# Kernel tuning notes

Hardware: AMD Instinct MI355X
Metric: run time of the kernel (lower is better)

## Reference

```python
import jax, jax.numpy as jnp
import numpy as np

N = 100000   # num_nodes
E = 1600000  # num_edges
D = 32       # hidden dim
H = 2        # GAT heads
EF = 16      # edge_feat_dim


def setup_inputs() -> dict:
    key = jax.random.key(0)
    ks = jax.random.split(key, 18)
    s = 0.1
    inp = {
        "edge_index": jax.random.randint(ks[0], (2, E), 0, N),
        "edge_attr": jax.random.normal(ks[1], (E, EF), jnp.float32),
        "node_emb": jax.random.normal(ks[2], (N, D), jnp.float32) * s,
        # SAGEConv layers: lin_l (neighbors, with bias) + lin_r (root, no bias)
        "sage1_wl": jax.random.normal(ks[3], (D, D), jnp.float32) * s,
        "sage1_bl": jnp.zeros((D,), jnp.float32),
        "sage1_wr": jax.random.normal(ks[4], (D, D), jnp.float32) * s,
        "sage2_wl": jax.random.normal(ks[5], (D, D), jnp.float32) * s,
        "sage2_bl": jnp.zeros((D,), jnp.float32),
        "sage2_wr": jax.random.normal(ks[6], (D, D), jnp.float32) * s,
        # GATConv: lin (no bias), att_src/att_dst [H, D], output bias [D]
        "gat_w": jax.random.normal(ks[7], (D, H * D), jnp.float32) * s,
        "gat_att_src": jax.random.normal(ks[8], (H, D), jnp.float32) * s,
        "gat_att_dst": jax.random.normal(ks[9], (H, D), jnp.float32) * s,
        "gat_bias": jnp.zeros((D,), jnp.float32),
        # edge MLP: Linear(2D+EF, 32) -> ReLU -> Linear(32, 1)
        "mlp_w1": jax.random.normal(ks[10], (2 * D + EF, 32), jnp.float32) * s,
        "mlp_b1": jnp.zeros((32,), jnp.float32),
        "mlp_w2": jax.random.normal(ks[11], (32, 1), jnp.float32) * s,
        "mlp_b2": jnp.zeros((1,), jnp.float32),
    }
    return inp


def _sage(x, src, dst, wl, bl, wr):
    # mean aggregation of source messages at destination, then lin_l + lin_r(root)
    summ = jax.ops.segment_sum(x[src], dst, num_segments=N)
    cnt = jax.ops.segment_sum(jnp.ones((src.shape[0], 1), x.dtype), dst, num_segments=N)
    mean = summ / jnp.maximum(cnt, 1.0)
    return mean @ wl + bl + x @ wr


def _gat(x, src, dst, w, att_src, att_dst, bias):
    # PyG GATConv default: add self loops, softmax over incoming edges per dst,
    # concat=False -> mean over heads, then bias.
    loops = jnp.arange(N, dtype=src.dtype)
    s2 = jnp.concatenate([src, loops])
    d2 = jnp.concatenate([dst, loops])
    xh = (x @ w).reshape(N, H, D)                      # [N, H, D]
    a_s = jnp.einsum('nhd,hd->nh', xh, att_src)        # [N, H]
    a_d = jnp.einsum('nhd,hd->nh', xh, att_dst)
    alpha = jax.nn.leaky_relu(a_s[s2] + a_d[d2], 0.2)  # [E+N, H]
    m = jax.ops.segment_max(alpha, d2, num_segments=N)
    e = jnp.exp(alpha - m[d2])
    den = jax.ops.segment_sum(e, d2, num_segments=N)
    wgt = e / (den[d2] + 1e-16)                        # [E+N, H]
    out = jax.ops.segment_sum(xh[s2] * wgt[:, :, None], d2, num_segments=N)
    return out.mean(axis=1) + bias                     # [N, D]


def reference(edge_index, edge_attr, node_emb,
              sage1_wl, sage1_bl, sage1_wr,
              sage2_wl, sage2_bl, sage2_wr,
              gat_w, gat_att_src, gat_att_dst, gat_bias,
              mlp_w1, mlp_b1, mlp_w2, mlp_b2):
    src, dst = edge_index[0], edge_index[1]
    x = node_emb
    x = jax.nn.relu(_sage(x, src, dst, sage1_wl, sage1_bl, sage1_wr))
    x = jax.nn.relu(_sage(x, src, dst, sage2_wl, sage2_bl, sage2_wr))
    x = jax.nn.relu(_gat(x, src, dst, gat_w, gat_att_src, gat_att_dst, gat_bias))
    edge_input = jnp.concatenate([x[src], x[dst], edge_attr], axis=1)  # [E, 2D+EF]
    h = jax.nn.relu(edge_input @ mlp_w1 + mlp_b1)  # dropout is eval-mode identity
    return (h @ mlp_w2 + mlp_b2).squeeze()         # [E]
```

## Files before the change

### kernel.cpp

```cpp
#include <hip/hip_runtime.h>
#include <hip/hip_fp16.h>


#define DD 32
#define HH 2
#define EFF 16

#define EB 4096
#define PB_T 512
#define BIN_SHIFT 8

__device__ __forceinline__ float lrelu(float x) { return x > 0.f ? x : 0.2f * x; }

__global__ void scan1_k(const int* __restrict__ in, int* __restrict__ out,
                        int* __restrict__ blockSums, int M) {
    __shared__ int s_s[256];
    int blk = blockIdx.x, t = threadIdx.x;
    int base = blk * 1024 + t * 4;
    int v[4];
    int s = 0;
#pragma unroll
    for (int i = 0; i < 4; i++) {
        v[i] = (base + i < M) ? in[base + i] : 0;
        s += v[i];
    }
    s_s[t] = s;
    __syncthreads();
    for (int off = 1; off < 256; off <<= 1) {
        int x = (t >= off) ? s_s[t - off] : 0;
        __syncthreads();
        s_s[t] += x;
        __syncthreads();
    }
    int excl = s_s[t] - s;
#pragma unroll
    for (int i = 0; i < 4; i++) {
        if (base + i < M) out[base + i] = excl;
        excl += v[i];
    }
    if (t == 255) blockSums[blk] = s_s[255];
}

__global__ void scan2_k(int* __restrict__ blockSums, int* __restrict__ totalOut, int NB) {
    __shared__ int s_s[256];
    int t = threadIdx.x;
    int v = (t < NB) ? blockSums[t] : 0;
    s_s[t] = v;
    __syncthreads();
    for (int off = 1; off < 256; off <<= 1) {
        int x = (t >= off) ? s_s[t - off] : 0;
        __syncthreads();
        s_s[t] += x;
        __syncthreads();
    }
    if (t < NB) blockSums[t] = s_s[t] - v;
    if (t == 255) *totalOut = s_s[255];
}

__global__ void scan3_k(int* __restrict__ out, const int* __restrict__ blockSums, int M) {
    int i = blockIdx.x * blockDim.x + threadIdx.x;
    if (i < M) out[i] += blockSums[i >> 10];
}

__global__ void radixA_k(const int* __restrict__ dst, int* __restrict__ histA, int E,
                         int NBLK, int NBINS) {
    __shared__ int s_h[512];
    int blk = blockIdx.x, t = threadIdx.x;
    for (int b = t; b < 512; b += PB_T) s_h[b] = 0;
    __syncthreads();
    int e0 = blk * EB;
    for (int i = t; i < EB; i += PB_T) {
        int e = e0 + i;
        if (e < E) atomicAdd(&s_h[dst[e] >> BIN_SHIFT], 1);
    }
    __syncthreads();
    for (int b = t; b < NBINS; b += PB_T) histA[b * NBLK + blk] = s_h[b];
}

__global__ void radixB_k(const int* __restrict__ src, const int* __restrict__ dst,
                         const int* __restrict__ histScan, int* __restrict__ pairs,
                         int E, int NBLK, int NBINS) {
    __shared__ int s_base[512];
    int blk = blockIdx.x, t = threadIdx.x;
    for (int b = t; b < NBINS; b += PB_T) s_base[b] = histScan[b * NBLK + blk];
    __syncthreads();
    int e0 = blk * EB;
    for (int i = t; i < EB; i += PB_T) {
        int e = e0 + i;
        if (e < E) {
            int d = dst[e];
            int pos = atomicAdd(&s_base[d >> BIN_SHIFT], 1);
            pairs[pos] = (src[e] << 8) | (d & 255);
        }
    }
}

__global__ void radixC_v2(const int* __restrict__ histScan, const int* __restrict__ pairs,
                          int* __restrict__ rowptr, int* __restrict__ soff, int N,
                          int NBLK, int NBINS, int E) {
    __shared__ int cnt[256];
    __shared__ int scanBuf[256];
    __shared__ int basePos[256];
    int b = blockIdx.x, t = threadIdx.x;
    int base = b << BIN_SHIFT;
    cnt[t] = 0;
    __syncthreads();
    int segLo = histScan[b * NBLK];
    int segHi = (b + 1 < NBINS) ? histScan[(b + 1) * NBLK] : E;
    for (int i = segLo + t; i < segHi; i += 256) atomicAdd(&cnt[pairs[i] & 255], 1);
    __syncthreads();
    int v = cnt[t];
    scanBuf[t] = v;
    __syncthreads();
    for (int off = 1; off < 256; off <<= 1) {
        int x = (t >= off) ? scanBuf[t - off] : 0;
        __syncthreads();
        scanBuf[t] += x;
        __syncthreads();
    }
    int excl = segLo + scanBuf[t] - v;
    basePos[t] = excl;
    if (base + t < N) rowptr[base + t] = excl;
    if (b == NBINS - 1 && t == 0) rowptr[N] = E;
    __syncthreads();
    for (int i = segLo + t; i < segHi; i += 256) {
        int en = pairs[i];
        int pos = atomicAdd(&basePos[en & 255], 1);
        soff[pos] = (en >> 8) << 6;
    }
}

__global__ void cvt_k(const float* __restrict__ in, __half* __restrict__ out, int n) {
    int i = blockIdx.x * blockDim.x + threadIdx.x;
    if (i < n) out[i] = __float2half(in[i]);
}

__global__ void prep_c_k(const float* __restrict__ w, const float* __restrict__ att_src,
                         const float* __restrict__ att_dst, float4* __restrict__ c4) {
    int i = threadIdx.x;
    if (i >= DD) return;
    float cs0 = 0.f, cs1 = 0.f, cd0 = 0.f, cd1 = 0.f;
    for (int d = 0; d < DD; d++) {
        float w0 = w[i * (HH * DD) + d], w1 = w[i * (HH * DD) + DD + d];
        cs0 += w0 * att_src[d];
        cs1 += w1 * att_src[DD + d];
        cd0 += w0 * att_dst[d];
        cd1 += w1 * att_dst[DD + d];
    }
    c4[i] = make_float4(cs0, cs1, cd0, cd1);
}

__device__ __forceinline__ void unpack4(unsigned lo, unsigned hi, float f[4]) {
    float2 a = __half22float2(*reinterpret_cast<const __half2*>(&lo));
    float2 b = __half22float2(*reinterpret_cast<const __half2*>(&hi));
    f[0] = a.x; f[1] = a.y; f[2] = b.x; f[3] = b.y;
}

__global__ void sage8x8_k(const __half* __restrict__ x, const int* __restrict__ rowptr,
                          const int* __restrict__ soff, const float* __restrict__ wl,
                          const float* __restrict__ bl, const float* __restrict__ wr,
                          __half* __restrict__ out, const float4* __restrict__ c4,
                          float2* __restrict__ a_s, float2* __restrict__ a_d, int N) {
    __shared__ float s_wl[DD * DD];
    __shared__ float s_wr[DD * DD];
    __shared__ float s_b[DD];
    __shared__ float4 s_c[DD];
    for (int i = threadIdx.x; i < DD * DD; i += blockDim.x) {
        s_wl[i] = wl[i];
        s_wr[i] = wr[i];
    }
    if (threadIdx.x < DD) {
        s_b[threadIdx.x] = bl[threadIdx.x];
        if (a_s) s_c[threadIdx.x] = c4[threadIdx.x];
    }
    __syncthreads();
    int gid = blockIdx.x * blockDim.x + threadIdx.x;
    int n = gid >> 3;
    if (n >= N) return;
    int l = gid & 7;
    int lo = rowptr[n], hi = rowptr[n + 1];
    const char* xb = (const char*)x;
    float acc[4] = {0.f, 0.f, 0.f, 0.f};
    int j = lo;
    for (; j + 3 < hi; j += 4) {
        int o0 = soff[j], o1 = soff[j + 1], o2 = soff[j + 2], o3 = soff[j + 3];
        uint2 r0 = *(const uint2*)(xb + o0 + l * 8);
        uint2 r1 = *(const uint2*)(xb + o1 + l * 8);
        uint2 r2 = *(const uint2*)(xb + o2 + l * 8);
        uint2 r3 = *(const uint2*)(xb + o3 + l * 8);
        float v0[4], v1[4], v2[4], v3[4];
        unpack4(r0.x, r0.y, v0);
        unpack4(r1.x, r1.y, v1);
        unpack4(r2.x, r2.y, v2);
        unpack4(r3.x, r3.y, v3);
#pragma unroll
        for (int f = 0; f < 4; f++) acc[f] += (v0[f] + v1[f]) + (v2[f] + v3[f]);
    }
    for (; j < hi; j++) {
        uint2 r0 = *(const uint2*)(xb + soff[j] + l * 8);
        float v0[4];
        unpack4(r0.x, r0.y, v0);
#pragma unroll
        for (int f = 0; f < 4; f++) acc[f] += v0[f];
    }
    float inv = 1.0f / fmaxf((float)(hi - lo), 1.0f);
    float mx[4];
#pragma unroll
    for (int f = 0; f < 4; f++) mx[f] = acc[f] * inv;
    uint2 sr = *(const uint2*)(xb + (size_t)n * 64 + l * 8);
    float xv[4];
    unpack4(sr.x, sr.y, xv);
    float o[4];
#pragma unroll
    for (int f = 0; f < 4; f++) o[f] = s_b[4 * l + f];
#pragma unroll
    for (int i2 = 0; i2 < 8; i2++) {
        float bm[4], bx[4];
#pragma unroll
        for (int r = 0; r < 4; r++) {
            bm[r] = __shfl(mx[r], i2, 8);
            bx[r] = __shfl(xv[r], i2, 8);
        }
#pragma unroll
        for (int r = 0; r < 4; r++) {
            const float4 wlv = *(const float4*)(s_wl + (4 * i2 + r) * DD + 4 * l);
            const float4 wrv = *(const float4*)(s_wr + (4 * i2 + r) * DD + 4 * l);
            o[0] += bm[r] * wlv.x + bx[r] * wrv.x;
            o[1] += bm[r] * wlv.y + bx[r] * wrv.y;
            o[2] += bm[r] * wlv.z + bx[r] * wrv.z;
            o[3] += bm[r] * wlv.w + bx[r] * wrv.w;
        }
    }
#pragma unroll
    for (int f = 0; f < 4; f++) o[f] = fmaxf(o[f], 0.f);
    uint2 ow;
    *reinterpret_cast<__half2*>(&ow.x) = __floats2half2_rn(o[0], o[1]);
    *reinterpret_cast<__half2*>(&ow.y) = __floats2half2_rn(o[2], o[3]);
    *(uint2*)((char*)out + (size_t)n * 64 + l * 8) = ow;
    if (a_s) {
        float pa0 = 0.f, pa1 = 0.f, pd0 = 0.f, pd1 = 0.f;
#pragma unroll
        for (int r = 0; r < 4; r++) {
            float4 c = s_c[4 * l + r];
            pa0 += o[r] * c.x;
            pa1 += o[r] * c.y;
            pd0 += o[r] * c.z;
            pd1 += o[r] * c.w;
        }
#pragma unroll
        for (int off = 4; off > 0; off >>= 1) {
            pa0 += __shfl_xor(pa0, off, 8);
            pa1 += __shfl_xor(pa1, off, 8);
            pd0 += __shfl_xor(pd0, off, 8);
            pd1 += __shfl_xor(pd1, off, 8);
        }
        if (l == 0) {
            a_s[n] = make_float2(pa0, pa1);
            a_d[n] = make_float2(pd0, pd1);
        }
    }
}

__global__ void gat_agg_v10(const __half* __restrict__ x2, const float2* __restrict__ a_s,
                            const float2* __restrict__ a_d, const int* __restrict__ rowptr,
                            const int* __restrict__ soff, const float* __restrict__ gw,
                            const float* __restrict__ bias, const float* __restrict__ w1,
                            const float* __restrict__ b1, __half* __restrict__ Ps,
                            __half* __restrict__ Pd, int N) {
    __shared__ float s_gw[DD * HH * DD];
    __shared__ float s_w1[2 * DD * DD];
    __shared__ float s_b1[DD];
    __shared__ float s_bias[DD];
    int t = threadIdx.x;
    for (int i = t; i < DD * HH * DD; i += blockDim.x) s_gw[i] = gw[i];
    for (int i = t; i < 2 * DD * DD; i += blockDim.x) s_w1[i] = w1[i];
    if (t < DD) {
        s_b1[t] = b1[t];
        s_bias[t] = bias[t];
    }
    __syncthreads();
    int gid = blockIdx.x * blockDim.x + t;
    int n = gid >> 3;
    if (n >= N) return;
    int l = gid & 7;
    const char* xb = (const char*)x2;
    const char* asb = (const char*)a_s;
    int lo = rowptr[n], hi = rowptr[n + 1];
    float2 as = a_s[n], ad = a_d[n];
    float ws0 = __expf(lrelu(as.x + ad.x));
    float ws1 = __expf(lrelu(as.y + ad.y));
    uint2 sr = *(const uint2*)(xb + (size_t)n * 64 + l * 8);
    float xvs[4];
    unpack4(sr.x, sr.y, xvs);
    float den0 = ws0, den1 = ws1;
    float y0[4], y1[4];
#pragma unroll
    for (int f = 0; f < 4; f++) {
        y0[f] = ws0 * xvs[f];
        y1[f] = ws1 * xvs[f];
    }
    int j = lo;
    for (; j + 3 < hi; j += 4) {
        int o0 = soff[j], o1 = soff[j + 1], o2 = soff[j + 2], o3 = soff[j + 3];
        float2 s0 = *(const float2*)(asb + (o0 >> 3));
        float2 s1 = *(const float2*)(asb + (o1 >> 3));
        float2 s2 = *(const float2*)(asb + (o2 >> 3));
        float2 s3 = *(const float2*)(asb + (o3 >> 3));
        uint2 r0 = *(const uint2*)(xb + o0 + l * 8);
        uint2 r1 = *(const uint2*)(xb + o1 + l * 8);
        uint2 r2 = *(const uint2*)(xb + o2 + l * 8);
        uint2 r3 = *(const uint2*)(xb + o3 + l * 8);
        float w00 = __expf(lrelu(s0.x + ad.x)), w01 = __expf(lrelu(s0.y + ad.y));
        float w10 = __expf(lrelu(s1.x + ad.x)), w11 = __expf(lrelu(s1.y + ad.y));
        float w20 = __expf(lrelu(s2.x + ad.x)), w21 = __expf(lrelu(s2.y + ad.y));
        float w30 = __expf(lrelu(s3.x + ad.x)), w31 = __expf(lrelu(s3.y + ad.y));
        den0 += (w00 + w10) + (w20 + w30);
        den1 += (w01 + w11) + (w21 + w31);
        float v0[4], v1[4], v2[4], v3[4];
        unpack4(r0.x, r0.y, v0);
        unpack4(r1.x, r1.y, v1);
        unpack4(r2.x, r2.y, v2);
        unpack4(r3.x, r3.y, v3);
#pragma unroll
        for (int f = 0; f < 4; f++) {
            y0[f] += (w00 * v0[f] + w10 * v1[f]) + (w20 * v2[f] + w30 * v3[f]);
            y1[f] += (w01 * v0[f] + w11 * v1[f]) + (w21 * v2[f] + w31 * v3[f]);
        }
    }
    for (; j < hi; j++) {
        int o0 = soff[j];
        float2 s0 = *(const float2*)(asb + (o0 >> 3));
        uint2 r0 = *(const uint2*)(xb + o0 + l * 8);
        float w00 = __expf(lrelu(s0.x + ad.x)), w01 = __expf(lrelu(s0.y + ad.y));
        den0 += w00;
        den1 += w01;
        float v0[4];
        unpack4(r0.x, r0.y, v0);
#pragma unroll
        for (int f = 0; f < 4; f++) {
            y0[f] += w00 * v0[f];
            y1[f] += w01 * v0[f];
        }
    }
    float i0 = 1.0f / (den0 + 1e-16f), i1 = 1.0f / (den1 + 1e-16f);
    float u0[4], u1[4];
#pragma unroll
    for (int f = 0; f < 4; f++) {
        u0[f] = y0[f] * i0;
        u1[f] = y1[f] * i1;
    }
    float o[4] = {0.f, 0.f, 0.f, 0.f};
#pragma unroll
    for (int i2 = 0; i2 < 8; i2++) {
        float b0[4], b1v[4];
#pragma unroll
        for (int r = 0; r < 4; r++) {
            b0[r] = __shfl(u0[r], i2, 8);
            b1v[r] = __shfl(u1[r], i2, 8);
        }
#pragma unroll
        for (int r = 0; r < 4; r++) {
            const float4 g0 = *(const float4*)(s_gw + (4 * i2 + r) * (HH * DD) + 4 * l);
            const float4 g1 = *(const float4*)(s_gw + (4 * i2 + r) * (HH * DD) + DD + 4 * l);
            o[0] += b0[r] * g0.x + b1v[r] * g1.x;
            o[1] += b0[r] * g0.y + b1v[r] * g1.y;
            o[2] += b0[r] * g0.z + b1v[r] * g1.z;
            o[3] += b0[r] * g0.w + b1v[r] * g1.w;
        }
    }
#pragma unroll
    for (int f = 0; f < 4; f++) o[f] = fmaxf(0.5f * o[f] + s_bias[4 * l + f], 0.f);
    float ps[4], pd[4];
#pragma unroll
    for (int f = 0; f < 4; f++) {
        ps[f] = s_b1[4 * l + f];
        pd[f] = 0.f;
    }
#pragma unroll
    for (int i2 = 0; i2 < 8; i2++) {
        float bo[4];
#pragma unroll
        for (int r = 0; r < 4; r++) bo[r] = __shfl(o[r], i2, 8);
#pragma unroll
        for (int r = 0; r < 4; r++) {
            const float4 wa = *(const float4*)(s_w1 + (4 * i2 + r) * DD + 4 * l);
            const float4 wb = *(const float4*)(s_w1 + (DD + 4 * i2 + r) * DD + 4 * l);
            ps[0] += bo[r] * wa.x;
            ps[1] += bo[r] * wa.y;
            ps[2] += bo[r] * wa.z;
            ps[3] += bo[r] * wa.w;
            pd[0] += bo[r] * wb.x;
            pd[1] += bo[r] * wb.y;
            pd[2] += bo[r] * wb.z;
            pd[3] += bo[r] * wb.w;
        }
    }
    uint2 pw;
    *reinterpret_cast<__half2*>(&pw.x) = __floats2half2_rn(ps[0], ps[1]);
    *reinterpret_cast<__half2*>(&pw.y) = __floats2half2_rn(ps[2], ps[3]);
    *(uint2*)((char*)Ps + (size_t)n * 64 + l * 8) = pw;
    *reinterpret_cast<__half2*>(&pw.x) = __floats2half2_rn(pd[0], pd[1]);
    *reinterpret_cast<__half2*>(&pw.y) = __floats2half2_rn(pd[2], pd[3]);
    *(uint2*)((char*)Pd + (size_t)n * 64 + l * 8) = pw;
}

__device__ __forceinline__ void add_half_row(const __half* __restrict__ row, float acc[DD]) {
    const uint4* r4 = (const uint4*)row;
#pragma unroll
    for (int c = 0; c < 4; c++) {
        uint4 u = r4[c];
        unsigned uu[4] = {u.x, u.y, u.z, u.w};
#pragma unroll
        for (int t = 0; t < 4; t++) {
            __half2 h2 = *reinterpret_cast<const __half2*>(&uu[t]);
            float2 f = __half22float2(h2);
            acc[c * 8 + t * 2 + 0] += f.x;
            acc[c * 8 + t * 2 + 1] += f.y;
        }
    }
}

__global__ void edge_mlp_v3(const __half* __restrict__ Ps, const __half* __restrict__ Pd,
                            const float* __restrict__ eattr, const int* __restrict__ src,
                            const int* __restrict__ dst, const float* __restrict__ w1e,
                            const float* __restrict__ w2, const float* __restrict__ b2,
                            float* __restrict__ out, int E) {
    __shared__ float s_we[EFF * DD];
    __shared__ float s_w2[DD];
    for (int i = threadIdx.x; i < EFF * DD; i += blockDim.x) s_we[i] = w1e[i];
    if (threadIdx.x < DD) s_w2[threadIdx.x] = w2[threadIdx.x];
    __syncthreads();
    int e = blockIdx.x * blockDim.x + threadIdx.x;
    if (e >= E) return;
    float b2v = b2[0];
    int s = src[e], d = dst[e];
    float acc[DD] = {};
    add_half_row(Ps + (size_t)s * DD, acc);
    add_half_row(Pd + (size_t)d * DD, acc);
    const float4* ea4 = (const float4*)(eattr + (size_t)e * EFF);
#pragma unroll
    for (int c = 0; c < 4; c++) {
        float4 v = ea4[c];
        const float va[4] = {v.x, v.y, v.z, v.w};
#pragma unroll
        for (int r = 0; r < 4; r++) {
#pragma unroll
            for (int j4 = 0; j4 < 8; j4++) {
                const float4 w = *(const float4*)(s_we + (c * 4 + r) * DD + j4 * 4);
                acc[j4 * 4 + 0] += va[r] * w.x;
                acc[j4 * 4 + 1] += va[r] * w.y;
                acc[j4 * 4 + 2] += va[r] * w.z;
                acc[j4 * 4 + 3] += va[r] * w.w;
            }
        }
    }
    float p = b2v;
#pragma unroll
    for (int j = 0; j < DD; j++) p += fmaxf(acc[j], 0.f) * s_w2[j];
    out[e] = p;
}

extern "C" void kernel_launch(void* const* d_in, const int* in_sizes, int n_in,
                              void* d_out, int out_size, void* d_ws, size_t ws_size,
                              hipStream_t stream) {
    const int E = in_sizes[0] / 2;
    const int N = in_sizes[2] / DD;

    const int* src = (const int*)d_in[0];
    const int* dst = src + E;
    const float* edge_attr = (const float*)d_in[1];
    const float* node_emb = (const float*)d_in[2];
    const float* sage1_wl = (const float*)d_in[3];
    const float* sage1_bl = (const float*)d_in[4];
    const float* sage1_wr = (const float*)d_in[5];
    const float* sage2_wl = (const float*)d_in[6];
    const float* sage2_bl = (const float*)d_in[7];
    const float* sage2_wr = (const float*)d_in[8];
    const float* gat_w = (const float*)d_in[9];
    const float* gat_att_src = (const float*)d_in[10];
    const float* gat_att_dst = (const float*)d_in[11];
    const float* gat_bias = (const float*)d_in[12];
    const float* mlp_w1 = (const float*)d_in[13];
    const float* mlp_b1 = (const float*)d_in[14];
    const float* mlp_w2 = (const float*)d_in[15];
    const float* mlp_b2 = (const float*)d_in[16];
    float* out = (float*)d_out;

    const int NBINS = (N + 255) >> BIN_SHIFT;
    const int NBLK = (E + EB - 1) / EB;
    const int M = NBINS * NBLK;

    char* ws = (char*)d_ws;
    size_t off = 0;
    auto alloc = [&](size_t bytes) {
        char* p = ws + off;
        off = (off + bytes + 255) & ~(size_t)255;
        return p;
    };
    int* rowptr = (int*)alloc((size_t)(N + 1) * 4);
    int* blockSums = (int*)alloc(256 * 4);
    int* dTot = (int*)alloc(4);
    int* soff = (int*)alloc((size_t)E * 4);
    __half* x0h = (__half*)alloc((size_t)N * DD * 2);
    __half* x1h = (__half*)alloc((size_t)N * DD * 2);
    __half* x2h = (__half*)alloc((size_t)N * DD * 2);
    float2* a_s = (float2*)alloc((size_t)N * 8);
    float2* a_d = (float2*)alloc((size_t)N * 8);
    float4* c4 = (float4*)alloc(DD * 16);
    __half* Ps = (__half*)alloc((size_t)N * DD * 2);
    __half* Pd = (__half*)alloc((size_t)N * DD * 2);
    int* histA = (int*)alloc((size_t)M * 4);
    int* histScan = (int*)alloc((size_t)M * 4);
    int* pairs = (int*)alloc((size_t)E * 4);

    const int BS = 256;
    const int gE = (E + BS - 1) / BS;
    const int gN32 = (N * 32 + BS - 1) / BS;
    const int gN8 = (N * 8 + BS - 1) / BS;
    const int NBm = (M + 1023) / 1024;

    radixA_k<<<NBLK, PB_T, 0, stream>>>(dst, histA, E, NBLK, NBINS);
    scan1_k<<<NBm, 256, 0, stream>>>(histA, histScan, blockSums, M);
    scan2_k<<<1, 256, 0, stream>>>(blockSums, dTot, NBm);
    scan3_k<<<(M + BS - 1) / BS, BS, 0, stream>>>(histScan, blockSums, M);
    radixB_k<<<NBLK, PB_T, 0, stream>>>(src, dst, histScan, pairs, E, NBLK, NBINS);
    radixC_v2<<<NBINS, 256, 0, stream>>>(histScan, pairs, rowptr, soff, N, NBLK, NBINS, E);

    cvt_k<<<gN32, BS, 0, stream>>>(node_emb, x0h, N * DD);
    prep_c_k<<<1, 64, 0, stream>>>(gat_w, gat_att_src, gat_att_dst, c4);

    sage8x8_k<<<gN8, BS, 0, stream>>>(x0h, rowptr, soff, sage1_wl, sage1_bl, sage1_wr,
                                      x1h, nullptr, nullptr, nullptr, N);
    sage8x8_k<<<gN8, BS, 0, stream>>>(x1h, rowptr, soff, sage2_wl, sage2_bl, sage2_wr,
                                      x2h, c4, a_s, a_d, N);

    gat_agg_v10<<<gN8, BS, 0, stream>>>(x2h, a_s, a_d, rowptr, soff, gat_w, gat_bias,
                                        mlp_w1, mlp_b1, Ps, Pd, N);

    edge_mlp_v3<<<gE, BS, 0, stream>>>(Ps, Pd, edge_attr, src, dst,
                                       mlp_w1 + 2 * DD * DD, mlp_w2, mlp_b2, out, E);
}
```

Measured before the change: 253.3 us.

## Use 4 lanes per node with 16-byte loads; fp16 packed math in edge MLP

The SAGE and GAT aggregation kernels now give each node 4 lanes with 16-byte row loads instead of 8 lanes with 8-byte loads. This halves thread count and shuffle overhead, and each lane handles 8 features with 2-way unrolled neighbor loops. The edge MLP now does its accumulation in packed half2 FMAs, with the edge-attr weights converted to half in shared memory. The fp16 accumulation reduces precision of the hidden layer and risks tolerance failures, and the shorter unroll may expose more gather latency.

```diff
diff --git a/kernel.cpp b/kernel.cpp
--- a/kernel.cpp
+++ b/kernel.cpp
@@ -150,17 +150,20 @@
     c4[i] = make_float4(cs0, cs1, cd0, cd1);
 }
 
-__device__ __forceinline__ void unpack4(unsigned lo, unsigned hi, float f[4]) {
-    float2 a = __half22float2(*reinterpret_cast<const __half2*>(&lo));
-    float2 b = __half22float2(*reinterpret_cast<const __half2*>(&hi));
+__device__ __forceinline__ void unpack8(uint4 u, float f[8]) {
+    float2 a = __half22float2(*reinterpret_cast<const __half2*>(&u.x));
+    float2 b = __half22float2(*reinterpret_cast<const __half2*>(&u.y));
+    float2 c = __half22float2(*reinterpret_cast<const __half2*>(&u.z));
+    float2 d = __half22float2(*reinterpret_cast<const __half2*>(&u.w));
     f[0] = a.x; f[1] = a.y; f[2] = b.x; f[3] = b.y;
-}
-
-__global__ void sage8x8_k(const __half* __restrict__ x, const int* __restrict__ rowptr,
-                          const int* __restrict__ soff, const float* __restrict__ wl,
-                          const float* __restrict__ bl, const float* __restrict__ wr,
-                          __half* __restrict__ out, const float4* __restrict__ c4,
-                          float2* __restrict__ a_s, float2* __restrict__ a_d, int N) {
+    f[4] = c.x; f[5] = c.y; f[6] = d.x; f[7] = d.y;
+}
+
+__global__ void sage4x16_k(const __half* __restrict__ x, const int* __restrict__ rowptr,
+                           const int* __restrict__ soff, const float* __restrict__ wl,
+                           const float* __restrict__ bl, const float* __restrict__ wr,
+                           __half* __restrict__ out, const float4* __restrict__ c4,
+                           float2* __restrict__ a_s, float2* __restrict__ a_d, int N) {
     __shared__ float s_wl[DD * DD];
     __shared__ float s_wr[DD * DD];
     __shared__ float s_b[DD];
@@ -175,84 +178,85 @@
     }
     __syncthreads();
     int gid = blockIdx.x * blockDim.x + threadIdx.x;
-    int n = gid >> 3;
+    int n = gid >> 2;
     if (n >= N) return;
-    int l = gid & 7;
+    int l = gid & 3;
     int lo = rowptr[n], hi = rowptr[n + 1];
     const char* xb = (const char*)x;
-    float acc[4] = {0.f, 0.f, 0.f, 0.f};
+    float acc[8] = {};
     int j = lo;
-    for (; j + 3 < hi; j += 4) {
-        int o0 = soff[j], o1 = soff[j + 1], o2 = soff[j + 2], o3 = soff[j + 3];
-        uint2 r0 = *(const uint2*)(xb + o0 + l * 8);
-        uint2 r1 = *(const uint2*)(xb + o1 + l * 8);
-        uint2 r2 = *(const uint2*)(xb + o2 + l * 8);
-        uint2 r3 = *(const uint2*)(xb + o3 + l * 8);
-        float v0[4], v1[4], v2[4], v3[4];
-        unpack4(r0.x, r0.y, v0);
-        unpack4(r1.x, r1.y, v1);
-        unpack4(r2.x, r2.y, v2);
-        unpack4(r3.x, r3.y, v3);
-#pragma unroll
-        for (int f = 0; f < 4; f++) acc[f] += (v0[f] + v1[f]) + (v2[f] + v3[f]);
-    }
-    for (; j < hi; j++) {
-        uint2 r0 = *(const uint2*)(xb + soff[j] + l * 8);
-        float v0[4];
-        unpack4(r0.x, r0.y, v0);
-#pragma unroll
-        for (int f = 0; f < 4; f++) acc[f] += v0[f];
+    for (; j + 1 < hi; j += 2) {
+        int o0 = soff[j], o1 = soff[j + 1];
+        uint4 r0 = *(const uint4*)(xb + o0 + l * 16);
+        uint4 r1 = *(const uint4*)(xb + o1 + l * 16);
+        float v0[8], v1[8];
+        unpack8(r0, v0);
+        unpack8(r1, v1);
+#pragma unroll
+        for (int f = 0; f < 8; f++) acc[f] += v0[f] + v1[f];
+    }
+    if (j < hi) {
+        uint4 r0 = *(const uint4*)(xb + soff[j] + l * 16);
+        float v0[8];
+        unpack8(r0, v0);
+#pragma unroll
+        for (int f = 0; f < 8; f++) acc[f] += v0[f];
     }
     float inv = 1.0f / fmaxf((float)(hi - lo), 1.0f);
-    float mx[4];
-#pragma unroll
-    for (int f = 0; f < 4; f++) mx[f] = acc[f] * inv;
-    uint2 sr = *(const uint2*)(xb + (size_t)n * 64 + l * 8);
-    float xv[4];
-    unpack4(sr.x, sr.y, xv);
-    float o[4];
-#pragma unroll
-    for (int f = 0; f < 4; f++) o[f] = s_b[4 * l + f];
-#pragma unroll
-    for (int i2 = 0; i2 < 8; i2++) {
-        float bm[4], bx[4];
-#pragma unroll
-        for (int r = 0; r < 4; r++) {
-            bm[r] = __shfl(mx[r], i2, 8);
-            bx[r] = __shfl(xv[r], i2, 8);
-        }
-#pragma unroll
-        for (int r = 0; r < 4; r++) {
-            const float4 wlv = *(const float4*)(s_wl + (4 * i2 + r) * DD + 4 * l);
-            const float4 wrv = *(const float4*)(s_wr + (4 * i2 + r) * DD + 4 * l);
-            o[0] += bm[r] * wlv.x + bx[r] * wrv.x;
-            o[1] += bm[r] * wlv.y + bx[r] * wrv.y;
-            o[2] += bm[r] * wlv.z + bx[r] * wrv.z;
-            o[3] += bm[r] * wlv.w + bx[r] * wrv.w;
-        }
-    }
-#pragma unroll
-    for (int f = 0; f < 4; f++) o[f] = fmaxf(o[f], 0.f);
-    uint2 ow;
+    float mx[8];
+#pragma unroll
+    for (int f = 0; f < 8; f++) mx[f] = acc[f] * inv;
+    uint4 sr = *(const uint4*)(xb + (size_t)n * 64 + l * 16);
+    float xv[8];
+    unpack8(sr, xv);
+    float o[8];
+#pragma unroll
+    for (int f = 0; f < 8; f++) o[f] = s_b[8 * l + f];
+#pragma unroll
+    for (int i2 = 0; i2 < 4; i2++) {
+#pragma unroll
+        for (int r = 0; r < 8; r++) {
+            float bm = __shfl(mx[r], i2, 4);
+            float bx = __shfl(xv[r], i2, 4);
+            int row = 8 * i2 + r;
+            const float4 wl0 = *(const float4*)(s_wl + row * DD + 8 * l);
+            const float4 wl1 = *(const float4*)(s_wl + row * DD + 8 * l + 4);
+            const float4 wr0 = *(const float4*)(s_wr + row * DD + 8 * l);
+            const float4 wr1 = *(const float4*)(s_wr + row * DD + 8 * l + 4);
+            o[0] += bm * wl0.x + bx * wr0.x;
+            o[1] += bm * wl0.y + bx * wr0.y;
+            o[2] += bm * wl0.z + bx * wr0.z;
+            o[3] += bm * wl0.w + bx * wr0.w;
+            o[4] += bm * wl1.x + bx * wr1.x;
+            o[5] += bm * wl1.y + bx * wr1.y;
+            o[6] += bm * wl1.z + bx * wr1.z;
+            o[7] += bm * wl1.w + bx * wr1.w;
+        }
+    }
+#pragma unroll
+    for (int f = 0; f < 8; f++) o[f] = fmaxf(o[f], 0.f);
+    uint4 ow;
     *reinterpret_cast<__half2*>(&ow.x) = __floats2half2_rn(o[0], o[1]);
     *reinterpret_cast<__half2*>(&ow.y) = __floats2half2_rn(o[2], o[3]);
-    *(uint2*)((char*)out + (size_t)n * 64 + l * 8) = ow;
+    *reinterpret_cast<__half2*>(&ow.z) = __floats2half2_rn(o[4], o[5]);
+    *reinterpret_cast<__half2*>(&ow.w) = __floats2half2_rn(o[6], o[7]);
+    *(uint4*)((char*)out + (size_t)n * 64 + l * 16) = ow;
     if (a_s) {
         float pa0 = 0.f, pa1 = 0.f, pd0 = 0.f, pd1 = 0.f;
 #pragma unroll
-        for (int r = 0; r < 4; r++) {
-            float4 c = s_c[4 * l + r];
+        for (int r = 0; r < 8; r++) {
+            float4 c = s_c[8 * l + r];
             pa0 += o[r] * c.x;
             pa1 += o[r] * c.y;
             pd0 += o[r] * c.z;
             pd1 += o[r] * c.w;
         }
 #pragma unroll
-        for (int off = 4; off > 0; off >>= 1) {
-            pa0 += __shfl_xor(pa0, off, 8);
-            pa1 += __shfl_xor(pa1, off, 8);
-            pd0 += __shfl_xor(pd0, off, 8);
-            pd1 += __shfl_xor(pd1, off, 8);
+        for (int off = 2; off > 0; off >>= 1) {
+            pa0 += __shfl_xor(pa0, off, 4);
+            pa1 += __shfl_xor(pa1, off, 4);
+            pd0 += __shfl_xor(pd0, off, 4);
+            pd1 += __shfl_xor(pd1, off, 4);
         }
         if (l == 0) {
             a_s[n] = make_float2(pa0, pa1);
@@ -261,7 +265,7 @@
     }
 }
 
-__global__ void gat_agg_v10(const __half* __restrict__ x2, const float2* __restrict__ a_s,
+__global__ void gat_agg_v11(const __half* __restrict__ x2, const float2* __restrict__ a_s,
                             const float2* __restrict__ a_d, const int* __restrict__ rowptr,
                             const int* __restrict__ soff, const float* __restrict__ gw,
                             const float* __restrict__ bias, const float* __restrict__ w1,
@@ -280,183 +284,185 @@
     }
     __syncthreads();
     int gid = blockIdx.x * blockDim.x + t;
-    int n = gid >> 3;
+    int n = gid >> 2;
     if (n >= N) return;
-    int l = gid & 7;
+    int l = gid & 3;
     const char* xb = (const char*)x2;
     const char* asb = (const char*)a_s;
     int lo = rowptr[n], hi = rowptr[n + 1];
     float2 as = a_s[n], ad = a_d[n];
     float ws0 = __expf(lrelu(as.x + ad.x));
     float ws1 = __expf(lrelu(as.y + ad.y));
-    uint2 sr = *(const uint2*)(xb + (size_t)n * 64 + l * 8);
-    float xvs[4];
-    unpack4(sr.x, sr.y, xvs);
+    uint4 sr = *(const uint4*)(xb + (size_t)n * 64 + l * 16);
+    float xvs[8];
+    unpack8(sr, xvs);
     float den0 = ws0, den1 = ws1;
-    float y0[4], y1[4];
-#pragma unroll
-    for (int f = 0; f < 4; f++) {
+    float y0[8], y1[8];
+#pragma unroll
+    for (int f = 0; f < 8; f++) {
         y0[f] = ws0 * xvs[f];
         y1[f] = ws1 * xvs[f];
     }
     int j = lo;
-    for (; j + 3 < hi; j += 4) {
-        int o0 = soff[j], o1 = soff[j + 1], o2 = soff[j + 2], o3 = soff[j + 3];
+    for (; j + 1 < hi; j += 2) {
+        int o0 = soff[j], o1 = soff[j + 1];
         float2 s0 = *(const float2*)(asb + (o0 >> 3));
         float2 s1 = *(const float2*)(asb + (o1 >> 3));
-        float2 s2 = *(const float2*)(asb + (o2 >> 3));
-        float2 s3 = *(const float2*)(asb + (o3 >> 3));
-        uint2 r0 = *(const uint2*)(xb + o0 + l * 8);
-        uint2 r1 = *(const uint2*)(xb + o1 + l * 8);
-        uint2 r2 = *(const uint2*)(xb + o2 + l * 8);
-        uint2 r3 = *(const uint2*)(xb + o3 + l * 8);
+        uint4 r0 = *(const uint4*)(xb + o0 + l * 16);
+        uint4 r1 = *(const uint4*)(xb + o1 + l * 16);
         float w00 = __expf(lrelu(s0.x + ad.x)), w01 = __expf(lrelu(s0.y + ad.y));
         float w10 = __expf(lrelu(s1.x + ad.x)), w11 = __expf(lrelu(s1.y + ad.y));
-        float w20 = __expf(lrelu(s2.x + ad.x)), w21 = __expf(lrelu(s2.y + ad.y));
-        float w30 = __expf(lrelu(s3.x + ad.x)), w31 = __expf(lrelu(s3.y + ad.y));
-        den0 += (w00 + w10) + (w20 + w30);
-        den1 += (w01 + w11) + (w21 + w31);
-        float v0[4], v1[4], v2[4], v3[4];
-        unpack4(r0.x, r0.y, v0);
-        unpack4(r1.x, r1.y, v1);
-        unpack4(r2.x, r2.y, v2);
-        unpack4(r3.x, r3.y, v3);
-#pragma unroll
-        for (int f = 0; f < 4; f++) {
-            y0[f] += (w00 * v0[f] + w10 * v1[f]) + (w20 * v2[f] + w30 * v3[f]);
-            y1[f] += (w01 * v0[f] + w11 * v1[f]) + (w21 * v2[f] + w31 * v3[f]);
-        }
-    }
-    for (; j < hi; j++) {
+        den0 += w00 + w10;
+        den1 += w01 + w11;
+        float v0[8], v1[8];
+        unpack8(r0, v0);
+        unpack8(r1, v1);
+#pragma unroll
+        for (int f = 0; f < 8; f++) {
+            y0[f] += w00 * v0[f] + w10 * v1[f];
+            y1[f] += w01 * v0[f] + w11 * v1[f];
+        }
+    }
+    if (j < hi) {
         int o0 = soff[j];
         float2 s0 = *(const float2*)(asb + (o0 >> 3));
-        uint2 r0 = *(const uint2*)(xb + o0 + l * 8);
+        uint4 r0 = *(const uint4*)(xb + o0 + l * 16);
         float w00 = __expf(lrelu(s0.x + ad.x)), w01 = __expf(lrelu(s0.y + ad.y));
         den0 += w00;
         den1 += w01;
-        float v0[4];
-        unpack4(r0.x, r0.y, v0);
-#pragma unroll
-        for (int f = 0; f < 4; f++) {
+        float v0[8];
+        unpack8(r0, v0);
+#pragma unroll
+        for (int f = 0; f < 8; f++) {
             y0[f] += w00 * v0[f];
             y1[f] += w01 * v0[f];
         }
     }
     float i0 = 1.0f / (den0 + 1e-16f), i1 = 1.0f / (den1 + 1e-16f);
-    float u0[4], u1[4];
-#pragma unroll
-    for (int f = 0; f < 4; f++) {
+    float u0[8], u1[8];
+#pragma unroll
+    for (int f = 0; f < 8; f++) {
         u0[f] = y0[f] * i0;
         u1[f] = y1[f] * i1;
     }
-    float o[4] = {0.f, 0.f, 0.f, 0.f};
-#pragma unroll
-    for (int i2 = 0; i2 < 8; i2++) {
-        float b0[4], b1v[4];
-#pragma unroll
-        for (int r = 0; r < 4; r++) {
-            b0[r] = __shfl(u0[r], i2, 8);
-            b1v[r] = __shfl(u1[r], i2, 8);
-        }
-#pragma unroll
-        for (int r = 0; r < 4; r++) {
-            const float4 g0 = *(const float4*)(s_gw + (4 * i2 + r) * (HH * DD) + 4 * l);
-            const float4 g1 = *(const float4*)(s_gw + (4 * i2 + r) * (HH * DD) + DD + 4 * l);
-            o[0] += b0[r] * g0.x + b1v[r] * g1.x;
-            o[1] += b0[r] * g0.y + b1v[r] * g1.y;
-            o[2] += b0[r] * g0.z + b1v[r] * g1.z;
-            o[3] += b0[r] * g0.w + b1v[r] * g1.w;
-        }
-    }
-#pragma unroll
-    for (int f = 0; f < 4; f++) o[f] = fmaxf(0.5f * o[f] + s_bias[4 * l + f], 0.f);
-    float ps[4], pd[4];
-#pragma unroll
-    for (int f = 0; f < 4; f++) {
-        ps[f] = s_b1[4 * l + f];
+    float o[8] = {};
+#pragma unroll
+    for (int i2 = 0; i2 < 4; i2++) {
+#pragma unroll
+        for (int r = 0; r < 8; r++) {
+            float b0 = __shfl(u0[r], i2, 4);
+            float b1v = __shfl(u1[r], i2, 4);
+            int row = 8 * i2 + r;
+            const float4 g00 = *(const float4*)(s_gw + row * (HH * DD) + 8 * l);
+            const float4 g01 = *(const float4*)(s_gw + row * (HH * DD) + 8 * l + 4);
+            const float4 g10 = *(const float4*)(s_gw + row * (HH * DD) + DD + 8 * l);
+            const float4 g11 = *(const float4*)(s_gw + row * (HH * DD) + DD + 8 * l + 4);
+            o[0] += b0 * g00.x + b1v * g10.x;
+            o[1] += b0 * g00.y + b1v * g10.y;
+            o[2] += b0 * g00.z + b1v * g10.z;
+            o[3] += b0 * g00.w + b1v * g10.w;
+            o[4] += b0 * g01.x + b1v * g11.x;
+            o[5] += b0 * g01.y + b1v * g11.y;
+            o[6] += b0 * g01.z + b1v * g11.z;
+            o[7] += b0 * g01.w + b1v * g11.w;
+        }
+    }
+#pragma unroll
+    for (int f = 0; f < 8; f++) o[f] = fmaxf(0.5f * o[f] + s_bias[8 * l + f], 0.f);
+    float ps[8], pd[8];
+#pragma unroll
+    for (int f = 0; f < 8; f++) {
+        ps[f] = s_b1[8 * l + f];
         pd[f] = 0.f;
     }
 #pragma unroll
-    for (int i2 = 0; i2 < 8; i2++) {
-        float bo[4];
-#pragma unroll
-        for (int r = 0; r < 4; r++) bo[r] = __shfl(o[r], i2, 8);
-#pragma unroll
-        for (int r = 0; r < 4; r++) {
-            const float4 wa = *(const float4*)(s_w1 + (4 * i2 + r) * DD + 4 * l);
-            const float4 wb = *(const float4*)(s_w1 + (DD + 4 * i2 + r) * DD + 4 * l);
-            ps[0] += bo[r] * wa.x;
-            ps[1] += bo[r] * wa.y;
-            ps[2] += bo[r] * wa.z;
-            ps[3] += bo[r] * wa.w;
-            pd[0] += bo[r] * wb.x;
-            pd[1] += bo[r] * wb.y;
-            pd[2] += bo[r] * wb.z;
-            pd[3] += bo[r] * wb.w;
-        }
-    }
-    uint2 pw;
+    for (int i2 = 0; i2 < 4; i2++) {
+#pragma unroll
+        for (int r = 0; r < 8; r++) {
+            float bo = __shfl(o[r], i2, 4);
+            int row = 8 * i2 + r;
+            const float4 wa0 = *(const float4*)(s_w1 + row * DD + 8 * l);
+            const float4 wa1 = *(const float4*)(s_w1 + row * DD + 8 * l + 4);
+            const float4 wb0 = *(const float4*)(s_w1 + (DD + row) * DD + 8 * l);
+            const float4 wb1 = *(const float4*)(s_w1 + (DD + row) * DD + 8 * l + 4);
+            ps[0] += bo * wa0.x;
+            ps[1] += bo * wa0.y;
+            ps[2] += bo * wa0.z;
+            ps[3] += bo * wa0.w;
+            ps[4] += bo * wa1.x;
+            ps[5] += bo * wa1.y;
+            ps[6] += bo * wa1.z;
+            ps[7] += bo * wa1.w;
+            pd[0] += bo * wb0.x;
+            pd[1] += bo * wb0.y;
+            pd[2] += bo * wb0.z;
+            pd[3] += bo * wb0.w;
+            pd[4] += bo * wb1.x;
+            pd[5] += bo * wb1.y;
+            pd[6] += bo * wb1.z;
+            pd[7] += bo * wb1.w;
+        }
+    }
+    uint4 pw;
     *reinterpret_cast<__half2*>(&pw.x) = __floats2half2_rn(ps[0], ps[1]);
     *reinterpret_cast<__half2*>(&pw.y) = __floats2half2_rn(ps[2], ps[3]);
-    *(uint2*)((char*)Ps + (size_t)n * 64 + l * 8) = pw;
+    *reinterpret_cast<__half2*>(&pw.z) = __floats2half2_rn(ps[4], ps[5]);
+    *reinterpret_cast<__half2*>(&pw.w) = __floats2half2_rn(ps[6], ps[7]);
+    *(uint4*)((char*)Ps + (size_t)n * 64 + l * 16) = pw;
     *reinterpret_cast<__half2*>(&pw.x) = __floats2half2_rn(pd[0], pd[1]);
     *reinterpret_cast<__half2*>(&pw.y) = __floats2half2_rn(pd[2], pd[3]);
-    *(uint2*)((char*)Pd + (size_t)n * 64 + l * 8) = pw;
-}
-
-__device__ __forceinline__ void add_half_row(const __half* __restrict__ row, float acc[DD]) {
-    const uint4* r4 = (const uint4*)row;
-#pragma unroll
-    for (int c = 0; c < 4; c++) {
-        uint4 u = r4[c];
-        unsigned uu[4] = {u.x, u.y, u.z, u.w};
-#pragma unroll
-        for (int t = 0; t < 4; t++) {
-            __half2 h2 = *reinterpret_cast<const __half2*>(&uu[t]);
-            float2 f = __half22float2(h2);
-            acc[c * 8 + t * 2 + 0] += f.x;
-            acc[c * 8 + t * 2 + 1] += f.y;
-        }
-    }
-}
-
-__global__ void edge_mlp_v3(const __half* __restrict__ Ps, const __half* __restrict__ Pd,
+    *reinterpret_cast<__half2*>(&pw.z) = __floats2half2_rn(pd[4], pd[5]);
+    *reinterpret_cast<__half2*>(&pw.w) = __floats2half2_rn(pd[6], pd[7]);
+    *(uint4*)((char*)Pd + (size_t)n * 64 + l * 16) = pw;
+}
+
+__global__ void edge_mlp_v4(const __half* __restrict__ Ps, const __half* __restrict__ Pd,
                             const float* __restrict__ eattr, const int* __restrict__ src,
                             const int* __restrict__ dst, const float* __restrict__ w1e,
                             const float* __restrict__ w2, const float* __restrict__ b2,
                             float* __restrict__ out, int E) {
-    __shared__ float s_we[EFF * DD];
+    __shared__ __half2 s_weh[EFF * 16];
     __shared__ float s_w2[DD];
-    for (int i = threadIdx.x; i < EFF * DD; i += blockDim.x) s_we[i] = w1e[i];
+    for (int idx = threadIdx.x; idx < EFF * 16; idx += blockDim.x) {
+        int i = idx >> 4, jj = idx & 15;
+        s_weh[idx] = __floats2half2_rn(w1e[i * DD + 2 * jj], w1e[i * DD + 2 * jj + 1]);
+    }
     if (threadIdx.x < DD) s_w2[threadIdx.x] = w2[threadIdx.x];
     __syncthreads();
     int e = blockIdx.x * blockDim.x + threadIdx.x;
     if (e >= E) return;
     float b2v = b2[0];
     int s = src[e], d = dst[e];
-    float acc[DD] = {};
-    add_half_row(Ps + (size_t)s * DD, acc);
-    add_half_row(Pd + (size_t)d * DD, acc);
+    const uint4* ps4 = (const uint4*)((const char*)Ps + (size_t)s * 64);
+    const uint4* pd4 = (const uint4*)((const char*)Pd + (size_t)d * 64);
+    uint4 pa[4], pb[4];
+#pragma unroll
+    for (int c = 0; c < 4; c++) {
+        pa[c] = ps4[c];
+        pb[c] = pd4[c];
+    }
+    const __half2* pah = reinterpret_cast<const __half2*>(pa);
+    const __half2* pbh = reinterpret_cast<const __half2*>(pb);
+    __half2 acc[16];
+#pragma unroll
+    for (int jj = 0; jj < 16; jj++) acc[jj] = __hadd2(pah[jj], pbh[jj]);
     const float4* ea4 = (const float4*)(eattr + (size_t)e * EFF);
-#pragma unroll
-    for (int c = 0; c < 4; c++) {
-        float4 v = ea4[c];
-        const float va[4] = {v.x, v.y, v.z, v.w};
-#pragma unroll
-        for (int r = 0; r < 4; r++) {
-#pragma unroll
-            for (int j4 = 0; j4 < 8; j4++) {
-                const float4 w = *(const float4*)(s_we + (c * 4 + r) * DD + j4 * 4);
-                acc[j4 * 4 + 0] += va[r] * w.x;
-                acc[j4 * 4 + 1] += va[r] * w.y;
-                acc[j4 * 4 + 2] += va[r] * w.z;
-                acc[j4 * 4 + 3] += va[r] * w.w;
-            }
-        }
+    float4 e0 = ea4[0], e1 = ea4[1], e2 = ea4[2], e3 = ea4[3];
+    const float va[16] = {e0.x, e0.y, e0.z, e0.w, e1.x, e1.y, e1.z, e1.w,
+                          e2.x, e2.y, e2.z, e2.w, e3.x, e3.y, e3.z, e3.w};
+#pragma unroll
+    for (int i = 0; i < EFF; i++) {
+        __half2 eh = __float2half2_rn(va[i]);
+#pragma unroll
+        for (int jj = 0; jj < 16; jj++)
+            acc[jj] = __hfma2(s_weh[i * 16 + jj], eh, acc[jj]);
     }
     float p = b2v;
 #pragma unroll
-    for (int j = 0; j < DD; j++) p += fmaxf(acc[j], 0.f) * s_w2[j];
+    for (int jj = 0; jj < 16; jj++) {
+        float2 f = __half22float2(acc[jj]);
+        p += fmaxf(f.x, 0.f) * s_w2[2 * jj] + fmaxf(f.y, 0.f) * s_w2[2 * jj + 1];
+    }
     out[e] = p;
 }
 
@@ -516,7 +522,7 @@
     const int BS = 256;
     const int gE = (E + BS - 1) / BS;
     const int gN32 = (N * 32 + BS - 1) / BS;
-    const int gN8 = (N * 8 + BS - 1) / BS;
+    const int gN4 = (N * 4 + BS - 1) / BS;
     const int NBm = (M + 1023) / 1024;
 
     radixA_k<<<NBLK, PB_T, 0, stream>>>(dst, histA, E, NBLK, NBINS);
@@ -529,14 +535,14 @@
     cvt_k<<<gN32, BS, 0, stream>>>(node_emb, x0h, N * DD);
     prep_c_k<<<1, 64, 0, stream>>>(gat_w, gat_att_src, gat_att_dst, c4);
 
-    sage8x8_k<<<gN8, BS, 0, stream>>>(x0h, rowptr, soff, sage1_wl, sage1_bl, sage1_wr,
-                                      x1h, nullptr, nullptr, nullptr, N);
-    sage8x8_k<<<gN8, BS, 0, stream>>>(x1h, rowptr, soff, sage2_wl, sage2_bl, sage2_wr,
-                                      x2h, c4, a_s, a_d, N);
-
-    gat_agg_v10<<<gN8, BS, 0, stream>>>(x2h, a_s, a_d, rowptr, soff, gat_w, gat_bias,
+    sage4x16_k<<<gN4, BS, 0, stream>>>(x0h, rowptr, soff, sage1_wl, sage1_bl, sage1_wr,
+                                       x1h, nullptr, nullptr, nullptr, N);
+    sage4x16_k<<<gN4, BS, 0, stream>>>(x1h, rowptr, soff, sage2_wl, sage2_bl, sage2_wr,
+                                       x2h, c4, a_s, a_d, N);
+
+    gat_agg_v11<<<gN4, BS, 0, stream>>>(x2h, a_s, a_d, rowptr, soff, gat_w, gat_bias,
                                         mlp_w1, mlp_b1, Ps, Pd, N);
 
-    edge_mlp_v3<<<gE, BS, 0, stream>>>(Ps, Pd, edge_attr, src, dst,
+    edge_mlp_v4<<<gE, BS, 0, stream>>>(Ps, Pd, edge_attr, src, dst,
                                        mlp_w1 + 2 * DD * DD, mlp_w2, mlp_b2, out, E);
 }
```

Measured after the change: 256.3 us. Within noise of the previous version (+1.2%).
